# Kernel tuning notes

Measured on AMD Instinct MI355X. Metric: run time of the kernel, lower is better.

The kernel has to match this reference:

```python
import jax, jax.numpy as jnp
import numpy as np

B = 8                                   # point clouds per batch
NS = [65536, 16384, 4096, 1024, 256]    # points per scale (stride-4 downsampling)
CS = [32, 64, 128, 256, 512]            # encoder channels per scale
K = 3
BN_EPS = 1e-5


def setup_inputs() -> dict:
    key = jax.random.key(0)
    ks = iter(jax.random.split(key, 64))
    inp = {}
    for i, (n, c) in enumerate(zip(NS, CS)):
        inp[f"p{i}"] = jax.random.uniform(next(ks), (n, 3), jnp.float32)
        inp[f"f{i}"] = jax.random.normal(next(ks), (n, c), jnp.float32)
        inp[f"b{i}"] = jnp.repeat(jnp.arange(B, dtype=jnp.int32), n // B)
    # FP stage mlps: a:(4->3) [768,256,256], b:(3->2) [384,128,128],
    #               c:(2->1) [192,64,64],   d:(1->0) [96,32,32]
    cfg = {"a": (CS[3] + CS[4], CS[3]), "b": (CS[2] + CS[3], CS[2]),
           "c": (CS[1] + CS[2], CS[1]), "d": (CS[0] + CS[1], CS[0])}
    for s, (cin, ch) in cfg.items():
        for j, ci in ((1, cin), (2, ch)):
            inp[f"w{s}{j}"] = jax.random.normal(next(ks), (ci, ch), jnp.float32) / float(np.sqrt(ci))
            inp[f"bias{s}{j}"] = jnp.zeros((ch,), jnp.float32)
            inp[f"g{s}{j}"] = jnp.ones((ch,), jnp.float32)
            inp[f"bt{s}{j}"] = jnp.zeros((ch,), jnp.float32)
    return inp


def _knn_interpolate(x2, p2, p1):
    """torch_geometric.nn.knn_interpolate with k=3; equal-sized sorted batches."""
    n1, n2, c = p1.shape[0] // B, p2.shape[0] // B, x2.shape[1]
    p1b, p2b = p1.reshape(B, n1, 3), p2.reshape(B, n2, 3)
    x2b = x2.reshape(B, n2, c)
    # squared dists via |a|^2 + |b|^2 - 2ab (avoids [B,n1,n2,3] temporary)
    d2 = (jnp.sum(p1b * p1b, -1)[:, :, None] + jnp.sum(p2b * p2b, -1)[:, None, :]
          - 2.0 * jnp.einsum('bnd,bmd->bnm', p1b, p2b))
    neg_d2, idx = jax.lax.top_k(-d2, K)              # [B, n1, K]
    w = 1.0 / jnp.maximum(-neg_d2, 1e-16)            # inverse squared distance
    gath = jax.vmap(lambda x, i: x[i])(x2b, idx)     # [B, n1, K, c]
    out = jnp.einsum('bnk,bnkc->bnc', w, gath) / jnp.sum(w, -1, keepdims=True)
    return out.reshape(B * n1, c)


def _lin_bn_relu(x, w, bias, gamma, beta):
    h = x @ w + bias
    mu = jnp.mean(h, 0)
    var = jnp.mean((h - mu) ** 2, 0)
    return jax.nn.relu((h - mu) * jax.lax.rsqrt(var + BN_EPS) * gamma + beta)


def _fp_stage(p_fine, f_fine, p_coarse, f_coarse, w1, b1, g1, bt1, w2, b2, g2, bt2):
    up = _knn_interpolate(f_coarse, p_coarse, p_fine)
    x = jnp.concatenate([f_fine, up], axis=1)
    x = _lin_bn_relu(x, w1, b1, g1, bt1)
    return _lin_bn_relu(x, w2, b2, g2, bt2)


def reference(p0, p1, p2, p3, p4, f0, f1, f2, f3, f4, b0, b1, b2, b3, b4,
              wa1, biasa1, ga1, bta1, wa2, biasa2, ga2, bta2,
              wb1, biasb1, gb1, btb1, wb2, biasb2, gb2, btb2,
              wc1, biasc1, gc1, btc1, wc2, biasc2, gc2, btc2,
              wd1, biasd1, gd1, btd1, wd2, biasd2, gd2, btd2):
    f3 = _fp_stage(p3, f3, p4, f4, wa1, biasa1, ga1, bta1, wa2, biasa2, ga2, bta2)
    f2 = _fp_stage(p2, f2, p3, f3, wb1, biasb1, gb1, btb1, wb2, biasb2, gb2, btb2)
    f1 = _fp_stage(p1, f1, p2, f2, wc1, biasc1, gc1, btc1, wc2, biasc2, gc2, btc2)
    f0 = _fp_stage(p0, f0, p1, f1, wd1, biasd1, gd1, btd1, wd2, biasd2, gd2, btd2)
    return f0
```

## Files before the change

### kernel.cpp

```cpp
#include <hip/hip_runtime.h>

#define BN_EPS 1e-5f

typedef unsigned short us;

__device__ __forceinline__ float bf2f(us u) {
    union { unsigned int i; float f; } v; v.i = ((unsigned int)u) << 16; return v.f;
}
__device__ __forceinline__ us f2bf(float f) {
    unsigned int x = __float_as_uint(f);
    x += 0x7fffu + ((x >> 16) & 1u);
    return (us)(x >> 16);
}
__device__ __forceinline__ float ldf(const void* p, size_t i, int f32) {
    return f32 ? ((const float*)p)[i] : bf2f(((const us*)p)[i]);
}

__global__ void detect_kernel(const unsigned int* __restrict__ g, int* __restrict__ flag) {
    if (threadIdx.x == 0 && blockIdx.x == 0)
        *flag = ((g[0] & 0xFFFFu) == 0u) ? 1 : 0;
}

template<int MODE, int FPB, int SPLIT, int N2>
__global__ __launch_bounds__(FPB * SPLIT)
void knn_up_kernel(
    const void* __restrict__ p_fine,
    const void* __restrict__ p_coarse,
    const void* __restrict__ f_coarse,
    const float* __restrict__ stats,
    const void* __restrict__ gamma,
    const void* __restrict__ beta,
    float inv_n2,
    float* __restrict__ up_out,
    const int* __restrict__ pf32,
    int n2pb, int c2)
{
    __shared__ __align__(16) float cpx[N2], cpy[N2], cpz[N2], cs2[N2];
    __shared__ float aff_a[256], aff_b[256];
    __shared__ float cand_d[FPB][3 * SPLIT];
    __shared__ int   cand_i[FPB][3 * SPLIT];
    __shared__ int   s_idx[FPB][3];
    __shared__ float s_w[FPB][3];

    const int f32 = *pf32;
    const int tid = threadIdx.x;
    const int cbase = blockIdx.y * n2pb;

    for (int j = tid; j < n2pb; j += FPB * SPLIT) {
        const size_t b = (size_t)(cbase + j) * 3;
        const float x = ldf(p_coarse, b + 0, f32);
        const float y = ldf(p_coarse, b + 1, f32);
        const float z = ldf(p_coarse, b + 2, f32);
        cpx[j] = x; cpy[j] = y; cpz[j] = z;
        cs2[j] = __fadd_rn(__fadd_rn(__fmul_rn(x, x), __fmul_rn(y, y)), __fmul_rn(z, z));
    }
    if (MODE == 1) {
        for (int c = tid; c < c2; c += FPB * SPLIT) {
            float mu  = stats[c] * inv_n2;
            float var = stats[c2 + c] * inv_n2 - mu * mu;
            float a = ldf(gamma, c, f32) * rsqrtf(var + BN_EPS);
            aff_a[c] = a;
            aff_b[c] = ldf(beta, c, f32) - mu * a;
        }
    }
    __syncthreads();

    {
        const int f = tid % FPB;
        const int s = tid / FPB;
        const int row = (blockIdx.y * gridDim.x + blockIdx.x) * FPB + f;
        const size_t b = (size_t)row * 3;
        const float px = ldf(p_fine, b + 0, f32);
        const float py = ldf(p_fine, b + 1, f32);
        const float pz = ldf(p_fine, b + 2, f32);
        const float s1 = __fadd_rn(__fadd_rn(__fmul_rn(px, px), __fmul_rn(py, py)),
                                   __fmul_rn(pz, pz));
        const int len = n2pb / SPLIT;
        const int jb = s * len;
        float t0 = 1e30f, t1 = 1e30f, t2 = 1e30f;
        int i0 = jb, i1 = jb, i2 = jb;
        for (int j = jb; j < jb + len; j += 4) {
            const float4 X = *(const float4*)&cpx[j];
            const float4 Y = *(const float4*)&cpy[j];
            const float4 Z = *(const float4*)&cpz[j];
            const float4 S = *(const float4*)&cs2[j];
            #pragma unroll
            for (int q = 0; q < 4; ++q) {
                const float qx = ((const float*)&X)[q];
                const float qy = ((const float*)&Y)[q];
                const float qz = ((const float*)&Z)[q];
                const float s2 = ((const float*)&S)[q];
                const float dot = fmaf(pz, qz, fmaf(py, qy, __fmul_rn(px, qx)));
                const float d = __fsub_rn(__fadd_rn(s1, s2), __fmul_rn(2.0f, dot));
                const int jj = j + q;
                const bool a0 = d < t0, a1 = d < t1, a2 = d < t2;
                t2 = a1 ? t1 : (a2 ? d : t2);  i2 = a1 ? i1 : (a2 ? jj : i2);
                t1 = a0 ? t0 : (a1 ? d : t1);  i1 = a0 ? i0 : (a1 ? jj : i1);
                t0 = a0 ? d  : t0;             i0 = a0 ? jj : i0;
            }
        }
        cand_d[f][s * 3 + 0] = t0;  cand_i[f][s * 3 + 0] = cbase + i0;
        cand_d[f][s * 3 + 1] = t1;  cand_i[f][s * 3 + 1] = cbase + i1;
        cand_d[f][s * 3 + 2] = t2;  cand_i[f][s * 3 + 2] = cbase + i2;
    }
    __syncthreads();

    if (tid < FPB) {
        const int f = tid;
        unsigned long long used = 0;
        #pragma unroll
        for (int k = 0; k < 3; ++k) {
            float bd = 1e38f; int bi = 0x7fffffff; int bq = 0;
            for (int q = 0; q < 3 * SPLIT; ++q) {
                if (used & (1ull << q)) continue;
                const float d = cand_d[f][q]; const int i = cand_i[f][q];
                if (d < bd || (d == bd && i < bi)) { bd = d; bi = i; bq = q; }
            }
            used |= 1ull << bq;
            s_idx[f][k] = bi;
            s_w[f][k] = __fdiv_rn(1.0f, fmaxf(bd, 1e-16f));
        }
    }
    __syncthreads();

    const int lane = tid & 63, wv = tid >> 6;
    const int nw = (FPB * SPLIT) / 64;
    for (int p = wv; p < FPB; p += nw) {
        const int row = (blockIdx.y * gridDim.x + blockIdx.x) * FPB + p;
        const int g0 = s_idx[p][0], g1 = s_idx[p][1], g2 = s_idx[p][2];
        const float w0 = s_w[p][0], w1 = s_w[p][1], w2 = s_w[p][2];
        const float den = __fadd_rn(__fadd_rn(w0, w1), w2);
        float* __restrict__ urow = up_out + (size_t)row * c2;
        for (int c = lane; c < c2; c += 64) {
            float v0, v1, v2;
            if (MODE == 0) {
                v0 = ldf(f_coarse, (size_t)g0 * c2 + c, f32);
                v1 = ldf(f_coarse, (size_t)g1 * c2 + c, f32);
                v2 = ldf(f_coarse, (size_t)g2 * c2 + c, f32);
            } else {
                const float* fc = (const float*)f_coarse;
                const float aa = aff_a[c], bb = aff_b[c];
                v0 = fmaxf(aa * fc[(size_t)g0 * c2 + c] + bb, 0.f);
                v1 = fmaxf(aa * fc[(size_t)g1 * c2 + c] + bb, 0.f);
                v2 = fmaxf(aa * fc[(size_t)g2 * c2 + c] + bb, 0.f);
            }
            const float num = fmaf(w2, v2, fmaf(w1, v1, __fmul_rn(w0, v0)));
            urow[c] = __fdiv_rn(num, den);
        }
    }
}

__global__ __launch_bounds__(256)
void gemm1_bn_kernel(const void* __restrict__ Ffine,
                     const float* __restrict__ Up,
                     const void* __restrict__ W,
                     const void* __restrict__ bias,
                     float* __restrict__ H,
                     float* __restrict__ stats_out,
                     const int* __restrict__ pf32,
                     int M, int c1, int c2, int N)
{
    __shared__ __align__(16) float As[16][68];
    __shared__ __align__(16) float Bs[16][68];
    __shared__ float s_sum[64], s_sq[64];

    const int f32 = *pf32;
    const int K = c1 + c2;
    const int tid = threadIdx.x;
    const int tx = tid & 15, ty = tid >> 4;
    const int n0 = blockIdx.x * 64, m0 = blockIdx.y * 64;

    if (tid < 64) { s_sum[tid] = 0.f; s_sq[tid] = 0.f; }

    const int a_m = tid >> 2;
    const int a_k = (tid & 3) << 2;
    const int b_k = tid >> 4;
    const int b_n = (tid & 15) << 2;
    const int row = m0 + a_m;

    float avp[4]; float4 bvp;
    {
        const int k = a_k;
        if (k < c1) {
            if (f32) {
                const float4 v = *(const float4*)((const float*)Ffine + (size_t)row * c1 + k);
                avp[0] = v.x; avp[1] = v.y; avp[2] = v.z; avp[3] = v.w;
            } else {
                const ushort4 u = *(const ushort4*)((const us*)Ffine + (size_t)row * c1 + k);
                avp[0] = bf2f(u.x); avp[1] = bf2f(u.y); avp[2] = bf2f(u.z); avp[3] = bf2f(u.w);
            }
        } else {
            const float4 v = *(const float4*)(Up + (size_t)row * c2 + (k - c1));
            avp[0] = v.x; avp[1] = v.y; avp[2] = v.z; avp[3] = v.w;
        }
        bvp = make_float4(0.f, 0.f, 0.f, 0.f);
        if (n0 + b_n < N) {
            const size_t wi = (size_t)b_k * N + (n0 + b_n);
            if (f32) bvp = *(const float4*)((const float*)W + wi);
            else {
                const ushort4 u = *(const ushort4*)((const us*)W + wi);
                bvp = make_float4(bf2f(u.x), bf2f(u.y), bf2f(u.z), bf2f(u.w));
            }
        }
    }

    float acc[4][4] = {};

    for (int k0 = 0; k0 < K; k0 += 16) {
        #pragma unroll
        for (int i = 0; i < 4; ++i) As[a_k + i][a_m] = avp[i];
        *(float4*)&Bs[b_k][b_n] = bvp;
        __syncthreads();

        float avn[4]; float4 bvn;
        const int kn = k0 + 16;
        if (kn < K) {
            const int k = kn + a_k;
            if (k < c1) {
                if (f32) {
                    const float4 v = *(const float4*)((const float*)Ffine + (size_t)row * c1 + k);
                    avn[0] = v.x; avn[1] = v.y; avn[2] = v.z; avn[3] = v.w;
                } else {
                    const ushort4 u = *(const ushort4*)((const us*)Ffine + (size_t)row * c1 + k);
                    avn[0] = bf2f(u.x); avn[1] = bf2f(u.y); avn[2] = bf2f(u.z); avn[3] = bf2f(u.w);
                }
            } else {
                const float4 v = *(const float4*)(Up + (size_t)row * c2 + (k - c1));
                avn[0] = v.x; avn[1] = v.y; avn[2] = v.z; avn[3] = v.w;
            }
            bvn = make_float4(0.f, 0.f, 0.f, 0.f);
            if (n0 + b_n < N) {
                const size_t wi = (size_t)(kn + b_k) * N + (n0 + b_n);
                if (f32) bvn = *(const float4*)((const float*)W + wi);
                else {
                    const ushort4 u = *(const ushort4*)((const us*)W + wi);
                    bvn = make_float4(bf2f(u.x), bf2f(u.y), bf2f(u.z), bf2f(u.w));
                }
            }
        }

        #pragma unroll
        for (int kk = 0; kk < 16; ++kk) {
            const float4 a4 = *(const float4*)&As[kk][ty << 2];
            const float4 b4 = *(const float4*)&Bs[kk][tx << 2];
            const float aarr[4] = {a4.x, a4.y, a4.z, a4.w};
            const float barr[4] = {b4.x, b4.y, b4.z, b4.w};
            #pragma unroll
            for (int i = 0; i < 4; ++i)
                #pragma unroll
                for (int j = 0; j < 4; ++j)
                    acc[i][j] = fmaf(aarr[i], barr[j], acc[i][j]);
        }
        __syncthreads();

        if (kn < K) {
            #pragma unroll
            for (int i = 0; i < 4; ++i) avp[i] = avn[i];
            bvp = bvn;
        }
    }

    float bvals[4];
    const bool colsok = (n0 + (tx << 2)) < N;
    #pragma unroll
    for (int j = 0; j < 4; ++j) {
        const int n = n0 + (tx << 2) + j;
        bvals[j] = (n < N) ? ldf(bias, n, f32) : 0.f;
    }
    float ps[4] = {0.f, 0.f, 0.f, 0.f}, pq[4] = {0.f, 0.f, 0.f, 0.f};
    #pragma unroll
    for (int i = 0; i < 4; ++i) {
        float4 hv;
        float* hvp = (float*)&hv;
        #pragma unroll
        for (int j = 0; j < 4; ++j) {
            const float v = acc[i][j] + bvals[j];
            hvp[j] = v;
            ps[j] += v;
            pq[j] = fmaf(v, v, pq[j]);
        }
        if (colsok)
            *(float4*)(H + (size_t)(m0 + (ty << 2) + i) * N + n0 + (tx << 2)) = hv;
    }
    #pragma unroll
    for (int j = 0; j < 4; ++j) {
        atomicAdd(&s_sum[(tx << 2) + j], ps[j]);
        atomicAdd(&s_sq[(tx << 2) + j], pq[j]);
    }
    __syncthreads();
    if (tid < 64) {
        const int n = n0 + tid;
        if (n < N) {
            atomicAdd(&stats_out[n], s_sum[tid]);
            atomicAdd(&stats_out[N + n], s_sq[tid]);
        }
    }
}

__global__ __launch_bounds__(256)
void gemm2_bn_kernel(const float* __restrict__ A,
                     const void* __restrict__ W,
                     const void* __restrict__ bias,
                     const float* __restrict__ stats_in,
                     const void* __restrict__ g_in,
                     const void* __restrict__ bt_in,
                     float inv_m,
                     float* __restrict__ H,
                     float* __restrict__ stats_out,
                     const int* __restrict__ pf32,
                     int M, int K, int N)
{
    __shared__ __align__(16) float As[16][68];
    __shared__ __align__(16) float Bs[16][68];
    __shared__ float aff_a[256], aff_b[256];
    __shared__ float s_sum[64], s_sq[64];

    const int f32 = *pf32;
    const int tid = threadIdx.x;
    const int tx = tid & 15, ty = tid >> 4;
    const int n0 = blockIdx.x * 64, m0 = blockIdx.y * 64;

    for (int c = tid; c < K; c += 256) {
        float mu  = stats_in[c] * inv_m;
        float var = stats_in[K + c] * inv_m - mu * mu;
        float a = ldf(g_in, c, f32) * rsqrtf(var + BN_EPS);
        aff_a[c] = a; aff_b[c] = ldf(bt_in, c, f32) - mu * a;
    }
    if (tid < 64) { s_sum[tid] = 0.f; s_sq[tid] = 0.f; }
    __syncthreads();

    const int a_m = tid >> 2;
    const int a_k = (tid & 3) << 2;
    const int b_k = tid >> 4;
    const int b_n = (tid & 15) << 2;
    const int row = m0 + a_m;

    float avp[4]; float4 bvp;
    {
        const float4 af = *(const float4*)(A + (size_t)row * K + a_k);
        avp[0] = af.x; avp[1] = af.y; avp[2] = af.z; avp[3] = af.w;
        bvp = make_float4(0.f, 0.f, 0.f, 0.f);
        if (n0 + b_n < N) {
            const size_t wi = (size_t)b_k * N + (n0 + b_n);
            if (f32) bvp = *(const float4*)((const float*)W + wi);
            else {
                const ushort4 u = *(const ushort4*)((const us*)W + wi);
                bvp = make_float4(bf2f(u.x), bf2f(u.y), bf2f(u.z), bf2f(u.w));
            }
        }
    }

    float acc[4][4] = {};

    for (int k0 = 0; k0 < K; k0 += 16) {
        #pragma unroll
        for (int i = 0; i < 4; ++i)
            As[a_k + i][a_m] = fmaxf(fmaf(aff_a[k0 + a_k + i], avp[i], aff_b[k0 + a_k + i]), 0.f);
        *(float4*)&Bs[b_k][b_n] = bvp;
        __syncthreads();

        float avn[4]; float4 bvn;
        const int kn = k0 + 16;
        if (kn < K) {
            const float4 af = *(const float4*)(A + (size_t)row * K + (kn + a_k));
            avn[0] = af.x; avn[1] = af.y; avn[2] = af.z; avn[3] = af.w;
            bvn = make_float4(0.f, 0.f, 0.f, 0.f);
            if (n0 + b_n < N) {
                const size_t wi = (size_t)(kn + b_k) * N + (n0 + b_n);
                if (f32) bvn = *(const float4*)((const float*)W + wi);
                else {
                    const ushort4 u = *(const ushort4*)((const us*)W + wi);
                    bvn = make_float4(bf2f(u.x), bf2f(u.y), bf2f(u.z), bf2f(u.w));
                }
            }
        }

        #pragma unroll
        for (int kk = 0; kk < 16; ++kk) {
            const float4 a4 = *(const float4*)&As[kk][ty << 2];
            const float4 b4 = *(const float4*)&Bs[kk][tx << 2];
            const float aarr[4] = {a4.x, a4.y, a4.z, a4.w};
            const float barr[4] = {b4.x, b4.y, b4.z, b4.w};
            #pragma unroll
            for (int i = 0; i < 4; ++i)
                #pragma unroll
                for (int j = 0; j < 4; ++j)
                    acc[i][j] = fmaf(aarr[i], barr[j], acc[i][j]);
        }
        __syncthreads();

        if (kn < K) {
            #pragma unroll
            for (int i = 0; i < 4; ++i) avp[i] = avn[i];
            bvp = bvn;
        }
    }

    float bvals[4];
    const bool colsok = (n0 + (tx << 2)) < N;
    #pragma unroll
    for (int j = 0; j < 4; ++j) {
        const int n = n0 + (tx << 2) + j;
        bvals[j] = (n < N) ? ldf(bias, n, f32) : 0.f;
    }
    float ps[4] = {0.f, 0.f, 0.f, 0.f}, pq[4] = {0.f, 0.f, 0.f, 0.f};
    #pragma unroll
    for (int i = 0; i < 4; ++i) {
        float4 hv;
        float* hvp = (float*)&hv;
        #pragma unroll
        for (int j = 0; j < 4; ++j) {
            const float v = acc[i][j] + bvals[j];
            hvp[j] = v;
            ps[j] += v;
            pq[j] = fmaf(v, v, pq[j]);
        }
        if (colsok)
            *(float4*)(H + (size_t)(m0 + (ty << 2) + i) * N + n0 + (tx << 2)) = hv;
    }
    #pragma unroll
    for (int j = 0; j < 4; ++j) {
        atomicAdd(&s_sum[(tx << 2) + j], ps[j]);
        atomicAdd(&s_sq[(tx << 2) + j], pq[j]);
    }
    __syncthreads();
    if (tid < 64) {
        const int n = n0 + tid;
        if (n < N) {
            atomicAdd(&stats_out[n], s_sum[tid]);
            atomicAdd(&stats_out[N + n], s_sq[tid]);
        }
    }
}

__global__ __launch_bounds__(256)
void finalize_kernel(const float* __restrict__ Hf, const float* __restrict__ stats,
                     const void* __restrict__ g, const void* __restrict__ bt,
                     float inv_m, void* __restrict__ out,
                     const int* __restrict__ pf32, int total)
{
    const int idx = blockIdx.x * 256 + threadIdx.x;
    if (idx >= total) return;
    const int f32 = *pf32;
    const int c = idx & 31;
    const float mu  = stats[c] * inv_m;
    const float var = stats[32 + c] * inv_m - mu * mu;
    const float a = ldf(g, c, f32) * rsqrtf(var + BN_EPS);
    const float b = ldf(bt, c, f32) - mu * a;
    const float v = fmaxf(fmaf(a, Hf[idx], b), 0.f);
    if (f32) ((float*)out)[idx] = v;
    else     ((us*)out)[idx] = f2bf(v);
}

extern "C" void kernel_launch(void* const* d_in, const int* in_sizes, int n_in,
                              void* d_out, int out_size, void* d_ws, size_t ws_size,
                              hipStream_t stream) {
    (void)in_sizes; (void)n_in; (void)out_size; (void)ws_size;
    const void* p0 = d_in[0];
    const void* f0 = d_in[1];
    const void* p1 = d_in[3];
    const void* f1 = d_in[4];
    const void* p2 = d_in[6];
    const void* f2 = d_in[7];
    const void* p3 = d_in[9];
    const void* f3 = d_in[10];
    const void* p4 = d_in[12];
    const void* f4 = d_in[13];
    const void *W1[4], *B1[4], *G1[4], *T1[4], *W2[4], *B2[4], *G2[4], *T2[4];
    for (int s = 0; s < 4; ++s) {
        const int b = 15 + s * 8;
        W1[s] = d_in[b + 0]; B1[s] = d_in[b + 1];
        G1[s] = d_in[b + 2]; T1[s] = d_in[b + 3];
        W2[s] = d_in[b + 4]; B2[s] = d_in[b + 5];
        G2[s] = d_in[b + 6]; T2[s] = d_in[b + 7];
    }

    float* stats = (float*)d_ws;
    float* st_a1 = stats + 0;
    float* st_a2 = stats + 512;
    float* st_b1 = stats + 1024;
    float* st_b2 = stats + 1280;
    float* st_c1 = stats + 1536;
    float* st_c2 = stats + 1664;
    float* st_d1 = stats + 1792;
    float* st_d2 = stats + 1856;
    int*   flag  = (int*)(stats + 1920);
    float* U = (float*)((char*)d_ws + 8192);
    float* H = U + 4194304;
    float* h2a = H + 262144;
    float* h2b = H + 524288;
    float* h2c = H + 1048576;
    float* h2d = U;

    hipMemsetAsync(d_ws, 0, 1920 * sizeof(float), stream);
    detect_kernel<<<1, 64, 0, stream>>>((const unsigned int*)G1[0], flag);

    knn_up_kernel<0, 64, 4, 32><<<dim3(2, 8), 256, 0, stream>>>(
        p3, p4, f4, nullptr, nullptr, nullptr, 0.f, U, flag, 32, 512);
    gemm1_bn_kernel<<<dim3(4, 16), 256, 0, stream>>>(
        f3, U, W1[0], B1[0], H, st_a1, flag, 1024, 256, 512, 256);
    gemm2_bn_kernel<<<dim3(4, 16), 256, 0, stream>>>(
        H, W2[0], B2[0], st_a1, G1[0], T1[0], 1.f / 1024.f,
        h2a, st_a2, flag, 1024, 256, 256);
    knn_up_kernel<1, 64, 4, 128><<<dim3(8, 8), 256, 0, stream>>>(
        p2, p3, h2a, st_a2, G2[0], T2[0], 1.f / 1024.f, U, flag, 128, 256);
    gemm1_bn_kernel<<<dim3(2, 64), 256, 0, stream>>>(
        f2, U, W1[1], B1[1], H, st_b1, flag, 4096, 128, 256, 128);
    gemm2_bn_kernel<<<dim3(2, 64), 256, 0, stream>>>(
        H, W2[1], B2[1], st_b1, G1[1], T1[1], 1.f / 4096.f,
        h2b, st_b2, flag, 4096, 128, 128);
    knn_up_kernel<1, 32, 16, 512><<<dim3(64, 8), 512, 0, stream>>>(
        p1, p2, h2b, st_b2, G2[1], T2[1], 1.f / 4096.f, U, flag, 512, 128);
    gemm1_bn_kernel<<<dim3(1, 256), 256, 0, stream>>>(
        f1, U, W1[2], B1[2], H, st_c1, flag, 16384, 64, 128, 64);
    gemm2_bn_kernel<<<dim3(1, 256), 256, 0, stream>>>(
        H, W2[2], B2[2], st_c1, G1[2], T1[2], 1.f / 16384.f,
        h2c, st_c2, flag, 16384, 64, 64);
    knn_up_kernel<1, 64, 8, 2048><<<dim3(128, 8), 512, 0, stream>>>(
        p0, p1, h2c, st_c2, G2[2], T2[2], 1.f / 16384.f, U, flag, 2048, 64);
    gemm1_bn_kernel<<<dim3(1, 1024), 256, 0, stream>>>(
        f0, U, W1[3], B1[3], H, st_d1, flag, 65536, 32, 64, 32);
    gemm2_bn_kernel<<<dim3(1, 1024), 256, 0, stream>>>(
        H, W2[3], B2[3], st_d1, G1[3], T1[3], 1.f / 65536.f,
        h2d, st_d2, flag, 65536, 32, 32);
    finalize_kernel<<<(65536 * 32) / 256, 256, 0, stream>>>(
        h2d, st_d2, G2[3], T2[3], 1.f / 65536.f, d_out, flag, 65536 * 32);
}
```

Measured before the change: 535.5 us.

## Merge per-split kNN candidates with wavefront shuffles and padded per-split LDS layout

```diff
diff --git a/kernel.cpp b/kernel.cpp
--- a/kernel.cpp
+++ b/kernel.cpp
@@ -19,6 +19,23 @@
 __global__ void detect_kernel(const unsigned int* __restrict__ g, int* __restrict__ flag) {
     if (threadIdx.x == 0 && blockIdx.x == 0)
         *flag = ((g[0] & 0xFFFFu) == 0u) ? 1 : 0;
+}
+
+__device__ __forceinline__ void lexmerge33(
+    const float a0, const int A0, const float a1, const int A1, const float a2, const int A2,
+    const float b0, const int B0, const float b1, const int B1, const float b2, const int B2,
+    float& m0, int& M0, float& m1, int& M1, float& m2, int& M2)
+{
+    const bool c1 = (a0 < b0) || (a0 == b0 && A0 < B0);
+    m0 = c1 ? a0 : b0;  M0 = c1 ? A0 : B0;
+    const float hAd = c1 ? a1 : a0;  const int hAi = c1 ? A1 : A0;
+    const float hBd = c1 ? b0 : b1;  const int hBi = c1 ? B0 : B1;
+    const bool c2 = (hAd < hBd) || (hAd == hBd && hAi < hBi);
+    m1 = c2 ? hAd : hBd;  M1 = c2 ? hAi : hBi;
+    const float gAd = c2 ? (c1 ? a2 : a1) : hAd;  const int gAi = c2 ? (c1 ? A2 : A1) : hAi;
+    const float gBd = c2 ? hBd : (c1 ? b1 : b2);  const int gBi = c2 ? hBi : (c1 ? B1 : B2);
+    const bool c3 = (gAd < gBd) || (gAd == gBd && gAi < gBi);
+    m2 = c3 ? gAd : gBd;  M2 = c3 ? gAi : gBi;
 }
 
 template<int MODE, int FPB, int SPLIT, int N2>
@@ -35,10 +52,13 @@
     const int* __restrict__ pf32,
     int n2pb, int c2)
 {
-    __shared__ __align__(16) float cpx[N2], cpy[N2], cpz[N2], cs2[N2];
+    constexpr int LEN = N2 / SPLIT;
+    constexpr int PSTR = LEN + 4;
+    __shared__ __align__(16) float cpx[SPLIT * PSTR];
+    __shared__ __align__(16) float cpy[SPLIT * PSTR];
+    __shared__ __align__(16) float cpz[SPLIT * PSTR];
+    __shared__ __align__(16) float cs2[SPLIT * PSTR];
     __shared__ float aff_a[256], aff_b[256];
-    __shared__ float cand_d[FPB][3 * SPLIT];
-    __shared__ int   cand_i[FPB][3 * SPLIT];
     __shared__ int   s_idx[FPB][3];
     __shared__ float s_w[FPB][3];
 
@@ -46,13 +66,14 @@
     const int tid = threadIdx.x;
     const int cbase = blockIdx.y * n2pb;
 
-    for (int j = tid; j < n2pb; j += FPB * SPLIT) {
+    for (int j = tid; j < N2; j += FPB * SPLIT) {
         const size_t b = (size_t)(cbase + j) * 3;
         const float x = ldf(p_coarse, b + 0, f32);
         const float y = ldf(p_coarse, b + 1, f32);
         const float z = ldf(p_coarse, b + 2, f32);
-        cpx[j] = x; cpy[j] = y; cpz[j] = z;
-        cs2[j] = __fadd_rn(__fadd_rn(__fmul_rn(x, x), __fmul_rn(y, y)), __fmul_rn(z, z));
+        const int pos = (j / LEN) * PSTR + (j & (LEN - 1));
+        cpx[pos] = x; cpy[pos] = y; cpz[pos] = z;
+        cs2[pos] = __fadd_rn(__fadd_rn(__fmul_rn(x, x), __fmul_rn(y, y)), __fmul_rn(z, z));
     }
     if (MODE == 1) {
         for (int c = tid; c < c2; c += FPB * SPLIT) {
@@ -66,8 +87,8 @@
     __syncthreads();
 
     {
-        const int f = tid % FPB;
-        const int s = tid / FPB;
+        const int f = tid / SPLIT;
+        const int s = tid & (SPLIT - 1);
         const int row = (blockIdx.y * gridDim.x + blockIdx.x) * FPB + f;
         const size_t b = (size_t)row * 3;
         const float px = ldf(p_fine, b + 0, f32);
@@ -75,15 +96,15 @@
         const float pz = ldf(p_fine, b + 2, f32);
         const float s1 = __fadd_rn(__fadd_rn(__fmul_rn(px, px), __fmul_rn(py, py)),
                                    __fmul_rn(pz, pz));
-        const int len = n2pb / SPLIT;
-        const int jb = s * len;
+        const int jb = s * LEN;
+        const int base = s * PSTR;
         float t0 = 1e30f, t1 = 1e30f, t2 = 1e30f;
         int i0 = jb, i1 = jb, i2 = jb;
-        for (int j = jb; j < jb + len; j += 4) {
-            const float4 X = *(const float4*)&cpx[j];
-            const float4 Y = *(const float4*)&cpy[j];
-            const float4 Z = *(const float4*)&cpz[j];
-            const float4 S = *(const float4*)&cs2[j];
+        for (int t = 0; t < LEN; t += 4) {
+            const float4 X = *(const float4*)&cpx[base + t];
+            const float4 Y = *(const float4*)&cpy[base + t];
+            const float4 Z = *(const float4*)&cpz[base + t];
+            const float4 S = *(const float4*)&cs2[base + t];
             #pragma unroll
             for (int q = 0; q < 4; ++q) {
                 const float qx = ((const float*)&X)[q];
@@ -92,33 +113,29 @@
                 const float s2 = ((const float*)&S)[q];
                 const float dot = fmaf(pz, qz, fmaf(py, qy, __fmul_rn(px, qx)));
                 const float d = __fsub_rn(__fadd_rn(s1, s2), __fmul_rn(2.0f, dot));
-                const int jj = j + q;
+                const int jj = jb + t + q;
                 const bool a0 = d < t0, a1 = d < t1, a2 = d < t2;
                 t2 = a1 ? t1 : (a2 ? d : t2);  i2 = a1 ? i1 : (a2 ? jj : i2);
                 t1 = a0 ? t0 : (a1 ? d : t1);  i1 = a0 ? i0 : (a1 ? jj : i1);
                 t0 = a0 ? d  : t0;             i0 = a0 ? jj : i0;
             }
         }
-        cand_d[f][s * 3 + 0] = t0;  cand_i[f][s * 3 + 0] = cbase + i0;
-        cand_d[f][s * 3 + 1] = t1;  cand_i[f][s * 3 + 1] = cbase + i1;
-        cand_d[f][s * 3 + 2] = t2;  cand_i[f][s * 3 + 2] = cbase + i2;
-    }
-    __syncthreads();
-
-    if (tid < FPB) {
-        const int f = tid;
-        unsigned long long used = 0;
-        #pragma unroll
-        for (int k = 0; k < 3; ++k) {
-            float bd = 1e38f; int bi = 0x7fffffff; int bq = 0;
-            for (int q = 0; q < 3 * SPLIT; ++q) {
-                if (used & (1ull << q)) continue;
-                const float d = cand_d[f][q]; const int i = cand_i[f][q];
-                if (d < bd || (d == bd && i < bi)) { bd = d; bi = i; bq = q; }
-            }
-            used |= 1ull << bq;
-            s_idx[f][k] = bi;
-            s_w[f][k] = __fdiv_rn(1.0f, fmaxf(bd, 1e-16f));
+
+        #pragma unroll
+        for (int m = 1; m < SPLIT; m <<= 1) {
+            const float o0 = __shfl_xor(t0, m, 64); const int oi0 = __shfl_xor(i0, m, 64);
+            const float o1 = __shfl_xor(t1, m, 64); const int oi1 = __shfl_xor(i1, m, 64);
+            const float o2 = __shfl_xor(t2, m, 64); const int oi2 = __shfl_xor(i2, m, 64);
+            float n0, n1, n2v; int ni0, ni1, ni2;
+            lexmerge33(t0, i0, t1, i1, t2, i2,
+                       o0, oi0, o1, oi1, o2, oi2,
+                       n0, ni0, n1, ni1, n2v, ni2);
+            t0 = n0; i0 = ni0; t1 = n1; i1 = ni1; t2 = n2v; i2 = ni2;
+        }
+        if (s == 0) {
+            s_idx[f][0] = cbase + i0;  s_w[f][0] = __fdiv_rn(1.0f, fmaxf(t0, 1e-16f));
+            s_idx[f][1] = cbase + i1;  s_w[f][1] = __fdiv_rn(1.0f, fmaxf(t1, 1e-16f));
+            s_idx[f][2] = cbase + i2;  s_w[f][2] = __fdiv_rn(1.0f, fmaxf(t2, 1e-16f));
         }
     }
     __syncthreads();
```

New measurement: 514.2 us. 4.0% less time.
